# Optimization experiments

Hardware: AMD Instinct MI355X
Metric: run time of the kernel (lower is better)

The kernel has to match this reference:

```python
import jax, jax.numpy as jnp
import numpy as np

VOCAB, EDIM, ENC, H, OUT = 50000, 128, 128, 100, 104
B, L, NPT = 128, 64, 64          # batch, statements per seq, nodes per statement tree
N = B * L * NPT                  # 524288 total nodes
MAXD = 6                         # max depth of a 64-node complete binary tree


def setup_inputs() -> dict:
    key = jax.random.key(0)
    ks = jax.random.split(key, 14)
    tokens = jax.random.randint(ks[0], (N,), 0, VOCAB)
    # structured tree topology: each statement tree is a 64-node complete binary tree
    local = np.arange(NPT)
    par_local = np.where(local == 0, 0, (local - 1) // 2)
    depth_local = np.floor(np.log2(local + 1)).astype(np.int32)
    base = np.repeat(np.arange(B * L) * NPT, NPT)
    parent = jnp.asarray(base + np.tile(par_local, B * L), dtype=jnp.int32)
    depth = jnp.asarray(np.tile(depth_local, B * L), dtype=jnp.int32)
    tree_id = jnp.asarray(np.repeat(np.arange(B * L), NPT), dtype=jnp.int32)
    nrm = lambda k, s, sc: jax.random.normal(k, s, jnp.float32) * sc
    return {
        "tokens": tokens, "parent": parent, "depth": depth, "tree_id": tree_id,
        "emb": nrm(ks[1], (VOCAB, EDIM), 0.02),
        "W_lin": nrm(ks[2], (ENC, EDIM), 0.05), "b_lin": nrm(ks[3], (ENC,), 0.05),
        "Wi_f": nrm(ks[4], (3 * H, ENC), 0.05), "Wh_f": nrm(ks[5], (3 * H, H), 0.05),
        "bi_f": nrm(ks[6], (3 * H,), 0.05), "bh_f": nrm(ks[7], (3 * H,), 0.05),
        "Wi_b": nrm(ks[8], (3 * H, ENC), 0.05), "Wh_b": nrm(ks[9], (3 * H, H), 0.05),
        "bi_b": nrm(ks[10], (3 * H,), 0.05), "bh_b": nrm(ks[11], (3 * H,), 0.05),
        "W_fc": nrm(ks[12], (OUT, 2 * H), 0.05), "b_fc": nrm(ks[13], (OUT,), 0.05),
    }


def _gru_scan(x_seq, Wi, Wh, bi, bh):
    # x_seq: [L, B, ENC] -> outputs [L, B, H]. Matches torch.nn.GRU cell math.
    def step(hprev, xt):
        gi = xt @ Wi.T + bi              # [B, 3H]
        gh = hprev @ Wh.T + bh
        ir, iz, inn = jnp.split(gi, 3, axis=-1)
        hr, hz, hn = jnp.split(gh, 3, axis=-1)
        r = jax.nn.sigmoid(ir + hr)
        z = jax.nn.sigmoid(iz + hz)
        n = jnp.tanh(inn + r * hn)
        hnew = (1.0 - z) * n + z * hprev
        return hnew, hnew
    h0 = jnp.zeros((x_seq.shape[1], Wh.shape[1]), x_seq.dtype)
    _, ys = jax.lax.scan(step, h0, x_seq)
    return ys


def reference(tokens, parent, depth, tree_id, emb, W_lin, b_lin,
              Wi_f, Wh_f, bi_f, bh_f, Wi_b, Wh_b, bi_b, bh_b, W_fc, b_fc):
    # per-node value: linear(embedding(token))   [N, ENC]
    h = emb[tokens] @ W_lin.T + b_lin
    # bottom-up subtree sum: h(node) = v(node) + sum(h(children)), batched by depth level
    for d in range(MAXD, 0, -1):
        contrib = jnp.where((depth == d)[:, None], h, 0.0)
        h = h.at[parent].add(contrib)
    # TreeEncoder output: max over all node hidden states of each tree
    encodes = jax.ops.segment_max(h, tree_id, num_segments=B * L)  # [B*L, ENC]
    x = encodes.reshape(B, L, ENC).transpose(1, 0, 2)              # [L, B, ENC]
    yf = _gru_scan(x, Wi_f, Wh_f, bi_f, bh_f)                      # [L, B, H]
    yb = _gru_scan(x[::-1], Wi_b, Wh_b, bi_b, bh_b)[::-1]
    gru_out = jnp.concatenate([yf, yb], axis=-1)                   # [L, B, 2H]
    pooled = gru_out.max(axis=0)                                   # [B, 2H]
    return pooled @ W_fc.T + b_fc                                  # [B, OUT]
```

## Files before the change

kernel.cpp:

```cpp
#include <hip/hip_runtime.h>
#include <hip/hip_bf16.h>

typedef __bf16 bf16_t;
typedef __attribute__((ext_vector_type(8))) __bf16 bf16x8;
typedef __attribute__((ext_vector_type(4))) float f32x4;

#define TREES 8192
#define ENC 128
#define HH 100
#define G3 300
#define GSTRIDE 304
#define BB 128
#define LL 64
#define OUTD 104
#define TPB_TREES 2

__device__ __forceinline__ float sigm(float x) { return 1.0f / (1.0f + __expf(-x)); }
__device__ __forceinline__ float tanh_f(float x) { return 2.0f / (1.0f + __expf(-2.0f * x)) - 1.0f; }

__device__ __forceinline__ int subtree_size(int n) {
  int np1 = n + 1;
  int d = 31 - __clz(np1);
  return ((64 >> d) - 1) + (((np1 & (np1 - 1)) == 0) ? 1 : 0);
}

__global__ __launch_bounds__(256) void k0_prep(const float* __restrict__ W_lin,
                                               const float* __restrict__ Wi_f,
                                               const float* __restrict__ Wi_b,
                                               bf16_t* __restrict__ Wbf,
                                               bf16_t* __restrict__ Wibf) {
  int i = blockIdx.x * 256 + threadIdx.x;
  if (i < 128 * 128) Wbf[i] = (bf16_t)W_lin[i];
  if (i < 608 * 128) {
    int jg = i >> 7, k = i & 127;
    int dir = (jg >= GSTRIDE) ? 1 : 0;
    int j = jg - dir * GSTRIDE;
    float v = 0.0f;
    if (j < G3) v = dir ? Wi_b[j * 128 + k] : Wi_f[j * 128 + k];
    Wibf[i] = (bf16_t)v;
  }
}

__global__ __launch_bounds__(256) void k1_tree(const int* __restrict__ tokens,
                                               const float* __restrict__ emb,
                                               const bf16_t* __restrict__ Wbf,
                                               const float* __restrict__ b_lin,
                                               float* __restrict__ encodes) {
  __shared__ float s[64][132];
  __shared__ bf16_t wl[128 * 136];
  __shared__ float maxbuf[4][128];
  __shared__ float sb[128];
  int tid = threadIdx.x;

  if (tid < 128) sb[tid] = b_lin[tid];

  {
    int row = tid >> 1;
    int half = tid & 1;
    const uint4* src = (const uint4*)(Wbf + row * 128 + half * 64);
    uint4* dst = (uint4*)(wl + row * 136 + half * 64);
#pragma unroll
    for (int i = 0; i < 8; ++i) dst[i] = src[i];
  }

  int wave = tid >> 6;
  int lane = tid & 63;
  int ri = lane & 15;
  int kg = lane >> 4;
  int m0 = wave * 16;
  float szs[4];
#pragma unroll
  for (int rr = 0; rr < 4; ++rr) szs[rr] = (float)subtree_size(m0 + kg * 4 + rr);

  for (int t = 0; t < TPB_TREES; ++t) {
    int tree = blockIdx.x * TPB_TREES + t;
    int base = tree * 64;

    {
      int n = tid >> 2;
      int q = tid & 3;
      int tok = tokens[base + n];
      const float4* src = (const float4*)(emb + (size_t)tok * ENC + q * 32);
#pragma unroll
      for (int i = 0; i < 8; ++i) {
        *(float4*)&s[n][q * 32 + i * 4] = src[i];
      }
    }
    __syncthreads();

    if (tid < 128) s[31][tid] += s[63][tid];
    __syncthreads();
    for (int lev = 4; lev >= 0; --lev) {
      int p0 = (1 << lev) - 1;
      int items = (1 << lev) * 128;
      for (int it = tid; it < items; it += 256) {
        int p = p0 + (it >> 7);
        int c = it & 127;
        s[p][c] += s[2 * p + 1][c] + s[2 * p + 2][c];
      }
      __syncthreads();
    }

    f32x4 acc[8];
#pragma unroll
    for (int nt = 0; nt < 8; ++nt) {
      f32x4 z = {0.f, 0.f, 0.f, 0.f};
      acc[nt] = z;
    }
#pragma unroll
    for (int ks = 0; ks < 4; ++ks) {
      int k0 = ks * 32 + kg * 8;
      float4 a0 = *(const float4*)&s[m0 + ri][k0];
      float4 a1 = *(const float4*)&s[m0 + ri][k0 + 4];
      bf16x8 afr;
      afr[0] = (bf16_t)a0.x; afr[1] = (bf16_t)a0.y; afr[2] = (bf16_t)a0.z; afr[3] = (bf16_t)a0.w;
      afr[4] = (bf16_t)a1.x; afr[5] = (bf16_t)a1.y; afr[6] = (bf16_t)a1.z; afr[7] = (bf16_t)a1.w;
#pragma unroll
      for (int nt = 0; nt < 8; ++nt) {
        bf16x8 bfr = *(const bf16x8*)&wl[(nt * 16 + ri) * 136 + k0];
        acc[nt] = __builtin_amdgcn_mfma_f32_16x16x32_bf16(afr, bfr, acc[nt], 0, 0, 0);
      }
    }
    float cmax[8];
#pragma unroll
    for (int nt = 0; nt < 8; ++nt) {
      float bl = sb[nt * 16 + ri];
      f32x4 a = acc[nt];
      a.x += szs[0] * bl;
      a.y += szs[1] * bl;
      a.z += szs[2] * bl;
      a.w += szs[3] * bl;
      cmax[nt] = fmaxf(fmaxf(a.x, a.y), fmaxf(a.z, a.w));
    }
#pragma unroll
    for (int off = 16; off < 64; off <<= 1) {
#pragma unroll
      for (int nt = 0; nt < 8; ++nt)
        cmax[nt] = fmaxf(cmax[nt], __shfl_xor(cmax[nt], off));
    }
    if (lane < 16) {
#pragma unroll
      for (int nt = 0; nt < 8; ++nt) maxbuf[wave][nt * 16 + lane] = cmax[nt];
    }
    __syncthreads();
    if (tid < 128) {
      float m = fmaxf(fmaxf(maxbuf[0][tid], maxbuf[1][tid]),
                      fmaxf(maxbuf[2][tid], maxbuf[3][tid]));
      encodes[(size_t)tree * ENC + tid] = m;
    }
    __syncthreads();
  }
}

__global__ __launch_bounds__(256) void k2_gi(const float* __restrict__ encodes,
                                             const bf16_t* __restrict__ Wibf,
                                             const float* __restrict__ bi_f,
                                             const float* __restrict__ bi_b,
                                             float* __restrict__ GI) {
  int tid = threadIdx.x;
  int wave = tid >> 6;
  int lane = tid & 63;
  int ri = lane & 15;
  int kg = lane >> 4;
  int m0 = blockIdx.x * 16;

  f32x4 acc[10];
#pragma unroll
  for (int i = 0; i < 10; ++i) {
    f32x4 z = {0.f, 0.f, 0.f, 0.f};
    acc[i] = z;
  }

  int r = m0 + ri;
  int er = (r & 127) * 64 + (r >> 7);
  const float* arow = encodes + (size_t)er * ENC;
#pragma unroll
  for (int ks = 0; ks < 4; ++ks) {
    int k0 = ks * 32 + kg * 8;
    float4 a0 = *(const float4*)(arow + k0);
    float4 a1 = *(const float4*)(arow + k0 + 4);
    bf16x8 afr;
    afr[0] = (bf16_t)a0.x; afr[1] = (bf16_t)a0.y; afr[2] = (bf16_t)a0.z; afr[3] = (bf16_t)a0.w;
    afr[4] = (bf16_t)a1.x; afr[5] = (bf16_t)a1.y; afr[6] = (bf16_t)a1.z; afr[7] = (bf16_t)a1.w;
#pragma unroll
    for (int i = 0; i < 10; ++i) {
      int nt = wave + i * 4;
      if (nt < 38) {
        bf16x8 bfr = *(const bf16x8*)(Wibf + (nt * 16 + ri) * 128 + k0);
        acc[i] = __builtin_amdgcn_mfma_f32_16x16x32_bf16(afr, bfr, acc[i], 0, 0, 0);
      }
    }
  }
#pragma unroll
  for (int i = 0; i < 10; ++i) {
    int nt = wave + i * 4;
    if (nt >= 38) continue;
    int jg = nt * 16 + ri;
    int dir = (jg >= GSTRIDE) ? 1 : 0;
    int j = jg - dir * GSTRIDE;
    if (j >= G3) continue;
    float bias = dir ? bi_b[j] : bi_f[j];
#pragma unroll
    for (int rr = 0; rr < 4; ++rr) {
      int rowg = m0 + kg * 4 + rr;
      int l = rowg >> 7, b = rowg & 127;
      GI[(((size_t)dir * LL + l) * BB + b) * GSTRIDE + j] = acc[i][rr] + bias;
    }
  }
}

__global__ __launch_bounds__(640) void k3_gru(const float* __restrict__ GI,
                                              const float* __restrict__ Wh_f,
                                              const float* __restrict__ Wh_b,
                                              const float* __restrict__ bh_f,
                                              const float* __restrict__ bh_b,
                                              float* __restrict__ pooled) {
  int blk = blockIdx.x;
  int dir = blk >> 7;
  int b = blk & 127;
  int tid = threadIdx.x;
  __shared__ __align__(16) float h_lds[104];
  __shared__ float gh_lds[304];
  __shared__ float gi_lds[2][304];
  const float* Wh = dir ? Wh_b : Wh_f;
  const float* bh = dir ? bh_b : bh_f;

  int j = tid >> 1;
  int kg = tid & 1;
  int kbase = kg * 52;
  bool isdot = (tid < 600);

  float4 wv[13];
  float bhj = 0.f;
  if (isdot) {
#pragma unroll
    for (int c = 0; c < 13; ++c) {
      int k0 = kbase + c * 4;
      float4 v;
      v.x = (k0 + 0 < HH) ? Wh[j * HH + k0 + 0] : 0.f;
      v.y = (k0 + 1 < HH) ? Wh[j * HH + k0 + 1] : 0.f;
      v.z = (k0 + 2 < HH) ? Wh[j * HH + k0 + 2] : 0.f;
      v.w = (k0 + 3 < HH) ? Wh[j * HH + k0 + 3] : 0.f;
      wv[c] = v;
    }
    if (kg == 0) bhj = bh[j];
  }
  if (tid < 104) h_lds[tid] = 0.f;

  const float* giB = GI + (size_t)dir * LL * BB * GSTRIDE + (size_t)b * GSTRIDE;
  if (tid < G3) {
    int la0 = dir ? 63 : 0;
    gi_lds[0][tid] = giB[(size_t)la0 * BB * GSTRIDE + tid];
  }
  float ymax = -1e30f;
  __syncthreads();

  for (int step = 0; step < 64; ++step) {
    int cur = step & 1;
    int nxt = cur ^ 1;
    float ginext = 0.f;
    if (tid < G3) {
      int ns = (step < 63) ? step + 1 : 63;
      int la = dir ? (63 - ns) : ns;
      ginext = giB[(size_t)la * BB * GSTRIDE + tid];
    }
    if (isdot) {
      float a0 = 0.f, a1 = 0.f, a2 = 0.f, a3 = 0.f;
#pragma unroll
      for (int c = 0; c < 13; ++c) {
        float4 hv = *(const float4*)&h_lds[kbase + c * 4];
        a0 += wv[c].x * hv.x;
        a1 += wv[c].y * hv.y;
        a2 += wv[c].z * hv.z;
        a3 += wv[c].w * hv.w;
      }
      float p = (a0 + a1) + (a2 + a3);
      p += __shfl_xor(p, 1);
      if (kg == 0) gh_lds[j] = p + bhj;
    }
    __syncthreads();
    if (tid < HH) {
      float r = sigm(gi_lds[cur][tid] + gh_lds[tid]);
      float z = sigm(gi_lds[cur][100 + tid] + gh_lds[100 + tid]);
      float n = tanh_f(gi_lds[cur][200 + tid] + r * gh_lds[200 + tid]);
      float hnew = (1.f - z) * n + z * h_lds[tid];
      ymax = fmaxf(ymax, hnew);
      h_lds[tid] = hnew;
    }
    if (tid < G3 && step < 63) gi_lds[nxt][tid] = ginext;
    __syncthreads();
  }
  if (tid < HH) pooled[(size_t)b * 200 + dir * 100 + tid] = ymax;
}

__global__ __launch_bounds__(128) void k4_fc(const float* __restrict__ pooled,
                                             const float* __restrict__ W_fc,
                                             const float* __restrict__ b_fc,
                                             float* __restrict__ out) {
  int b = blockIdx.x;
  int o = threadIdx.x;
  if (o >= OUTD) return;
  const float* p = pooled + (size_t)b * 200;
  const float* w = W_fc + (size_t)o * 200;
  float acc = b_fc[o];
#pragma unroll 8
  for (int j = 0; j < 200; ++j) acc += p[j] * w[j];
  out[(size_t)b * OUTD + o] = acc;
}

extern "C" void kernel_launch(void* const* d_in, const int* in_sizes, int n_in,
                              void* d_out, int out_size, void* d_ws, size_t ws_size,
                              hipStream_t stream) {
  const int* tokens = (const int*)d_in[0];
  const float* emb = (const float*)d_in[4];
  const float* W_lin = (const float*)d_in[5];
  const float* b_lin = (const float*)d_in[6];
  const float* Wi_f = (const float*)d_in[7];
  const float* Wh_f = (const float*)d_in[8];
  const float* bi_f = (const float*)d_in[9];
  const float* bh_f = (const float*)d_in[10];
  const float* Wi_b = (const float*)d_in[11];
  const float* Wh_b = (const float*)d_in[12];
  const float* bi_b = (const float*)d_in[13];
  const float* bh_b = (const float*)d_in[14];
  const float* W_fc = (const float*)d_in[15];
  const float* b_fc = (const float*)d_in[16];

  float* encodes = (float*)d_ws;
  float* GI = encodes + (size_t)TREES * ENC;
  float* pooled = GI + (size_t)2 * LL * BB * GSTRIDE;
  bf16_t* Wbf = (bf16_t*)(pooled + (size_t)BB * 200);
  bf16_t* Wibf = Wbf + 128 * 128;

  k0_prep<<<304, 256, 0, stream>>>(W_lin, Wi_f, Wi_b, Wbf, Wibf);
  k1_tree<<<TREES / TPB_TREES, 256, 0, stream>>>(tokens, emb, Wbf, b_lin, encodes);
  k2_gi<<<512, 256, 0, stream>>>(encodes, Wibf, bi_f, bi_b, GI);
  k3_gru<<<256, 640, 0, stream>>>(GI, Wh_f, Wh_b, bh_f, bh_b, pooled);
  k4_fc<<<BB, 128, 0, stream>>>(pooled, W_fc, b_fc, (float*)d_out);
}
```

Measured before the change: 172.2 us.

## Drop LDS weight staging, prefetch next tree embeddings, retile MFMA as 2x2 waves

The tree kernel no longer copies the bf16 linear weight into shared memory. Each wave now reads its B fragments straight from global memory (L2/L1). This cuts LDS use per block and adds a launch-bounds occupancy hint of 4 blocks. The embedding rows for the next tree are prefetched into registers while the current tree is reduced. The MFMA work is split as 2 row-halves by 2 column-halves across waves, which halves the max buffer. The trade-off is repeated global weight loads per tree and more register pressure from the prefetch buffer.

```diff
diff --git a/kernel.cpp b/kernel.cpp
--- a/kernel.cpp
+++ b/kernel.cpp
@@ -41,52 +41,56 @@
   }
 }
 
-__global__ __launch_bounds__(256) void k1_tree(const int* __restrict__ tokens,
-                                               const float* __restrict__ emb,
-                                               const bf16_t* __restrict__ Wbf,
-                                               const float* __restrict__ b_lin,
-                                               float* __restrict__ encodes) {
+__global__ __launch_bounds__(256, 4) void k1_tree(const int* __restrict__ tokens,
+                                                  const float* __restrict__ emb,
+                                                  const bf16_t* __restrict__ Wbf,
+                                                  const float* __restrict__ b_lin,
+                                                  float* __restrict__ encodes) {
   __shared__ float s[64][132];
-  __shared__ bf16_t wl[128 * 136];
-  __shared__ float maxbuf[4][128];
+  __shared__ float maxbuf[2][128];
   __shared__ float sb[128];
   int tid = threadIdx.x;
-
-  if (tid < 128) sb[tid] = b_lin[tid];
-
-  {
-    int row = tid >> 1;
-    int half = tid & 1;
-    const uint4* src = (const uint4*)(Wbf + row * 128 + half * 64);
-    uint4* dst = (uint4*)(wl + row * 136 + half * 64);
-#pragma unroll
-    for (int i = 0; i < 8; ++i) dst[i] = src[i];
-  }
-
   int wave = tid >> 6;
   int lane = tid & 63;
   int ri = lane & 15;
   int kg = lane >> 4;
-  int m0 = wave * 16;
-  float szs[4];
-#pragma unroll
-  for (int rr = 0; rr < 4; ++rr) szs[rr] = (float)subtree_size(m0 + kg * 4 + rr);
+  int wm = wave >> 1;
+  int wn = wave & 1;
+
+  if (tid < 128) sb[tid] = b_lin[tid];
+
+  int n = tid >> 2;
+  int q = tid & 3;
+  int tree0 = blockIdx.x * TPB_TREES;
+
+  float4 pre[8];
+  {
+    int tok = tokens[tree0 * 64 + n];
+    const float4* src = (const float4*)(emb + (size_t)tok * ENC + q * 32);
+#pragma unroll
+    for (int i = 0; i < 8; ++i) pre[i] = src[i];
+  }
+
+  float szs[2][4];
+#pragma unroll
+  for (int mi = 0; mi < 2; ++mi)
+#pragma unroll
+    for (int rr = 0; rr < 4; ++rr)
+      szs[mi][rr] = (float)subtree_size(wm * 32 + mi * 16 + kg * 4 + rr);
 
   for (int t = 0; t < TPB_TREES; ++t) {
-    int tree = blockIdx.x * TPB_TREES + t;
-    int base = tree * 64;
-
-    {
-      int n = tid >> 2;
-      int q = tid & 3;
-      int tok = tokens[base + n];
+    int tree = tree0 + t;
+
+#pragma unroll
+    for (int i = 0; i < 8; ++i) *(float4*)&s[n][q * 32 + i * 4] = pre[i];
+    __syncthreads();
+
+    if (t + 1 < TPB_TREES) {
+      int tok = tokens[(tree + 1) * 64 + n];
       const float4* src = (const float4*)(emb + (size_t)tok * ENC + q * 32);
 #pragma unroll
-      for (int i = 0; i < 8; ++i) {
-        *(float4*)&s[n][q * 32 + i * 4] = src[i];
-      }
-    }
-    __syncthreads();
+      for (int i = 0; i < 8; ++i) pre[i] = src[i];
+    }
 
     if (tid < 128) s[31][tid] += s[63][tid];
     __syncthreads();
@@ -101,52 +105,60 @@
       __syncthreads();
     }
 
-    f32x4 acc[8];
-#pragma unroll
-    for (int nt = 0; nt < 8; ++nt) {
-      f32x4 z = {0.f, 0.f, 0.f, 0.f};
-      acc[nt] = z;
-    }
+    f32x4 acc[2][4];
+#pragma unroll
+    for (int mi = 0; mi < 2; ++mi)
+#pragma unroll
+      for (int ni = 0; ni < 4; ++ni) {
+        f32x4 z = {0.f, 0.f, 0.f, 0.f};
+        acc[mi][ni] = z;
+      }
 #pragma unroll
     for (int ks = 0; ks < 4; ++ks) {
       int k0 = ks * 32 + kg * 8;
-      float4 a0 = *(const float4*)&s[m0 + ri][k0];
-      float4 a1 = *(const float4*)&s[m0 + ri][k0 + 4];
-      bf16x8 afr;
-      afr[0] = (bf16_t)a0.x; afr[1] = (bf16_t)a0.y; afr[2] = (bf16_t)a0.z; afr[3] = (bf16_t)a0.w;
-      afr[4] = (bf16_t)a1.x; afr[5] = (bf16_t)a1.y; afr[6] = (bf16_t)a1.z; afr[7] = (bf16_t)a1.w;
-#pragma unroll
-      for (int nt = 0; nt < 8; ++nt) {
-        bf16x8 bfr = *(const bf16x8*)&wl[(nt * 16 + ri) * 136 + k0];
-        acc[nt] = __builtin_amdgcn_mfma_f32_16x16x32_bf16(afr, bfr, acc[nt], 0, 0, 0);
-      }
-    }
-    float cmax[8];
-#pragma unroll
-    for (int nt = 0; nt < 8; ++nt) {
-      float bl = sb[nt * 16 + ri];
-      f32x4 a = acc[nt];
-      a.x += szs[0] * bl;
-      a.y += szs[1] * bl;
-      a.z += szs[2] * bl;
-      a.w += szs[3] * bl;
-      cmax[nt] = fmaxf(fmaxf(a.x, a.y), fmaxf(a.z, a.w));
+      bf16x8 bfr[4];
+#pragma unroll
+      for (int ni = 0; ni < 4; ++ni)
+        bfr[ni] = *(const bf16x8*)(Wbf + (size_t)((wn * 4 + ni) * 16 + ri) * 128 + k0);
+#pragma unroll
+      for (int mi = 0; mi < 2; ++mi) {
+        float4 a0 = *(const float4*)&s[wm * 32 + mi * 16 + ri][k0];
+        float4 a1 = *(const float4*)&s[wm * 32 + mi * 16 + ri][k0 + 4];
+        bf16x8 afr;
+        afr[0] = (bf16_t)a0.x; afr[1] = (bf16_t)a0.y; afr[2] = (bf16_t)a0.z; afr[3] = (bf16_t)a0.w;
+        afr[4] = (bf16_t)a1.x; afr[5] = (bf16_t)a1.y; afr[6] = (bf16_t)a1.z; afr[7] = (bf16_t)a1.w;
+#pragma unroll
+        for (int ni = 0; ni < 4; ++ni)
+          acc[mi][ni] = __builtin_amdgcn_mfma_f32_16x16x32_bf16(afr, bfr[ni], acc[mi][ni], 0, 0, 0);
+      }
+    }
+
+    float cmax[4];
+#pragma unroll
+    for (int ni = 0; ni < 4; ++ni) {
+      float bl = sb[(wn * 4 + ni) * 16 + ri];
+      float m = -1e30f;
+#pragma unroll
+      for (int mi = 0; mi < 2; ++mi) {
+        f32x4 a = acc[mi][ni];
+        m = fmaxf(m, fmaxf(fmaxf(a.x + szs[mi][0] * bl, a.y + szs[mi][1] * bl),
+                           fmaxf(a.z + szs[mi][2] * bl, a.w + szs[mi][3] * bl)));
+      }
+      cmax[ni] = m;
     }
 #pragma unroll
     for (int off = 16; off < 64; off <<= 1) {
 #pragma unroll
-      for (int nt = 0; nt < 8; ++nt)
-        cmax[nt] = fmaxf(cmax[nt], __shfl_xor(cmax[nt], off));
+      for (int ni = 0; ni < 4; ++ni)
+        cmax[ni] = fmaxf(cmax[ni], __shfl_xor(cmax[ni], off));
     }
     if (lane < 16) {
 #pragma unroll
-      for (int nt = 0; nt < 8; ++nt) maxbuf[wave][nt * 16 + lane] = cmax[nt];
+      for (int ni = 0; ni < 4; ++ni) maxbuf[wm][(wn * 4 + ni) * 16 + lane] = cmax[ni];
     }
     __syncthreads();
     if (tid < 128) {
-      float m = fmaxf(fmaxf(maxbuf[0][tid], maxbuf[1][tid]),
-                      fmaxf(maxbuf[2][tid], maxbuf[3][tid]));
-      encodes[(size_t)tree * ENC + tid] = m;
+      encodes[(size_t)tree * ENC + tid] = fmaxf(maxbuf[0][tid], maxbuf[1][tid]);
     }
     __syncthreads();
   }
```

Result: slower. 233.9 us (+35.8%).

## Map one tree per wave with register-resident subtree sums and no block syncs

Applied to the files above, without the earlier changes.

The tree kernel now gives each wavefront a whole tree. Embedding rows are gathered into 64 float2 registers per lane, and the bottom-up subtree sum runs entirely in registers instead of through shared memory with block barriers. Node values are packed to bf16 into a small per-wave swizzled LDS tile in 16-node chunks for the MFMA. W_lin fragments are read straight from global memory instead of being staged in LDS. This removes the block-wide __syncthreads and cuts LDS footprint. The cost is heavy register pressure (128 floats of node data per lane), which may reduce occupancy or cause spills.

```diff
diff --git a/kernel.cpp b/kernel.cpp
--- a/kernel.cpp
+++ b/kernel.cpp
@@ -13,7 +13,6 @@
 #define BB 128
 #define LL 64
 #define OUTD 104
-#define TPB_TREES 2
 
 __device__ __forceinline__ float sigm(float x) { return 1.0f / (1.0f + __expf(-x)); }
 __device__ __forceinline__ float tanh_f(float x) { return 2.0f / (1.0f + __expf(-2.0f * x)) - 1.0f; }
@@ -46,61 +45,52 @@
                                                const bf16_t* __restrict__ Wbf,
                                                const float* __restrict__ b_lin,
                                                float* __restrict__ encodes) {
-  __shared__ float s[64][132];
-  __shared__ bf16_t wl[128 * 136];
-  __shared__ float maxbuf[4][128];
-  __shared__ float sb[128];
+  __shared__ bf16_t tb[4][16 * 128];
   int tid = threadIdx.x;
-
-  if (tid < 128) sb[tid] = b_lin[tid];
-
-  {
-    int row = tid >> 1;
-    int half = tid & 1;
-    const uint4* src = (const uint4*)(Wbf + row * 128 + half * 64);
-    uint4* dst = (uint4*)(wl + row * 136 + half * 64);
-#pragma unroll
-    for (int i = 0; i < 8; ++i) dst[i] = src[i];
-  }
-
-  int wave = tid >> 6;
+  int wv = tid >> 6;
   int lane = tid & 63;
   int ri = lane & 15;
   int kg = lane >> 4;
-  int m0 = wave * 16;
-  float szs[4];
-#pragma unroll
-  for (int rr = 0; rr < 4; ++rr) szs[rr] = (float)subtree_size(m0 + kg * 4 + rr);
-
-  for (int t = 0; t < TPB_TREES; ++t) {
-    int tree = blockIdx.x * TPB_TREES + t;
-    int base = tree * 64;
-
-    {
-      int n = tid >> 2;
-      int q = tid & 3;
-      int tok = tokens[base + n];
-      const float4* src = (const float4*)(emb + (size_t)tok * ENC + q * 32);
-#pragma unroll
-      for (int i = 0; i < 8; ++i) {
-        *(float4*)&s[n][q * 32 + i * 4] = src[i];
-      }
-    }
-    __syncthreads();
-
-    if (tid < 128) s[31][tid] += s[63][tid];
-    __syncthreads();
-    for (int lev = 4; lev >= 0; --lev) {
-      int p0 = (1 << lev) - 1;
-      int items = (1 << lev) * 128;
-      for (int it = tid; it < items; it += 256) {
-        int p = p0 + (it >> 7);
-        int c = it & 127;
-        s[p][c] += s[2 * p + 1][c] + s[2 * p + 2][c];
-      }
-      __syncthreads();
-    }
-
+  int tree = blockIdx.x * 4 + wv;
+  bf16_t* T = &tb[wv][0];
+
+  float bl[8];
+#pragma unroll
+  for (int nt = 0; nt < 8; ++nt) bl[nt] = b_lin[nt * 16 + ri];
+
+  int tok = tokens[tree * 64 + lane];
+
+  float2 v[64];
+#pragma unroll
+  for (int n = 0; n < 64; ++n) {
+    int tk = __builtin_amdgcn_readlane(tok, n);
+    const float2* row = (const float2*)(emb + (size_t)tk * ENC);
+    v[n] = row[lane];
+  }
+
+  v[31].x += v[63].x; v[31].y += v[63].y;
+#pragma unroll
+  for (int p = 30; p >= 0; --p) {
+    v[p].x += v[2 * p + 1].x + v[2 * p + 2].x;
+    v[p].y += v[2 * p + 1].y + v[2 * p + 2].y;
+  }
+
+  float cmax[8];
+#pragma unroll
+  for (int nt = 0; nt < 8; ++nt) cmax[nt] = -1e30f;
+
+#pragma unroll
+  for (int ch = 0; ch < 4; ++ch) {
+#pragma unroll
+    for (int nc = 0; nc < 16; ++nc) {
+      float2 x = v[ch * 16 + nc];
+      unsigned int lo = (unsigned int)__builtin_bit_cast(unsigned short, (bf16_t)x.x);
+      unsigned int hi = (unsigned int)__builtin_bit_cast(unsigned short, (bf16_t)x.y);
+      unsigned int pk = (hi << 16) | lo;
+      int blk = (lane >> 2) ^ (nc & 7);
+      int col = (blk << 3) + ((2 * lane) & 7);
+      *(unsigned int*)(T + nc * 128 + col) = pk;
+    }
     f32x4 acc[8];
 #pragma unroll
     for (int nt = 0; nt < 8; ++nt) {
@@ -109,46 +99,36 @@
     }
 #pragma unroll
     for (int ks = 0; ks < 4; ++ks) {
-      int k0 = ks * 32 + kg * 8;
-      float4 a0 = *(const float4*)&s[m0 + ri][k0];
-      float4 a1 = *(const float4*)&s[m0 + ri][k0 + 4];
-      bf16x8 afr;
-      afr[0] = (bf16_t)a0.x; afr[1] = (bf16_t)a0.y; afr[2] = (bf16_t)a0.z; afr[3] = (bf16_t)a0.w;
-      afr[4] = (bf16_t)a1.x; afr[5] = (bf16_t)a1.y; afr[6] = (bf16_t)a1.z; afr[7] = (bf16_t)a1.w;
+      int b = ks * 4 + kg;
+      int rb = b ^ (ri & 7);
+      bf16x8 afr = *(const bf16x8*)(T + ri * 128 + rb * 8);
 #pragma unroll
       for (int nt = 0; nt < 8; ++nt) {
-        bf16x8 bfr = *(const bf16x8*)&wl[(nt * 16 + ri) * 136 + k0];
+        bf16x8 bfr = *(const bf16x8*)(Wbf + (size_t)(nt * 16 + ri) * 128 + ks * 32 + kg * 8);
         acc[nt] = __builtin_amdgcn_mfma_f32_16x16x32_bf16(afr, bfr, acc[nt], 0, 0, 0);
       }
     }
-    float cmax[8];
+    float szs[4];
+#pragma unroll
+    for (int rr = 0; rr < 4; ++rr) szs[rr] = (float)subtree_size(ch * 16 + kg * 4 + rr);
 #pragma unroll
     for (int nt = 0; nt < 8; ++nt) {
-      float bl = sb[nt * 16 + ri];
       f32x4 a = acc[nt];
-      a.x += szs[0] * bl;
-      a.y += szs[1] * bl;
-      a.z += szs[2] * bl;
-      a.w += szs[3] * bl;
-      cmax[nt] = fmaxf(fmaxf(a.x, a.y), fmaxf(a.z, a.w));
-    }
-#pragma unroll
-    for (int off = 16; off < 64; off <<= 1) {
-#pragma unroll
-      for (int nt = 0; nt < 8; ++nt)
-        cmax[nt] = fmaxf(cmax[nt], __shfl_xor(cmax[nt], off));
-    }
-    if (lane < 16) {
-#pragma unroll
-      for (int nt = 0; nt < 8; ++nt) maxbuf[wave][nt * 16 + lane] = cmax[nt];
-    }
-    __syncthreads();
-    if (tid < 128) {
-      float m = fmaxf(fmaxf(maxbuf[0][tid], maxbuf[1][tid]),
-                      fmaxf(maxbuf[2][tid], maxbuf[3][tid]));
-      encodes[(size_t)tree * ENC + tid] = m;
-    }
-    __syncthreads();
+      float m = fmaxf(fmaxf(a.x + szs[0] * bl[nt], a.y + szs[1] * bl[nt]),
+                      fmaxf(a.z + szs[2] * bl[nt], a.w + szs[3] * bl[nt]));
+      cmax[nt] = fmaxf(cmax[nt], m);
+    }
+  }
+#pragma unroll
+  for (int off = 16; off < 64; off <<= 1) {
+#pragma unroll
+    for (int nt = 0; nt < 8; ++nt)
+      cmax[nt] = fmaxf(cmax[nt], __shfl_xor(cmax[nt], off));
+  }
+  if (lane < 16) {
+#pragma unroll
+    for (int nt = 0; nt < 8; ++nt)
+      encodes[(size_t)tree * ENC + nt * 16 + lane] = cmax[nt];
   }
 }
 
@@ -333,7 +313,7 @@
   bf16_t* Wibf = Wbf + 128 * 128;
 
   k0_prep<<<304, 256, 0, stream>>>(W_lin, Wi_f, Wi_b, Wbf, Wibf);
-  k1_tree<<<TREES / TPB_TREES, 256, 0, stream>>>(tokens, emb, Wbf, b_lin, encodes);
+  k1_tree<<<TREES / 4, 256, 0, stream>>>(tokens, emb, Wbf, b_lin, encodes);
   k2_gi<<<512, 256, 0, stream>>>(encodes, Wibf, bi_f, bi_b, GI);
   k3_gru<<<256, 640, 0, stream>>>(GI, Wh_f, Wh_b, bh_f, bh_b, pooled);
   k4_fc<<<BB, 128, 0, stream>>>(pooled, W_fc, b_fc, (float*)d_out);
```

Measured after the change: 254.7 us. 47.9% more time.
